# Kernel tuning notes

Hardware: AMD Instinct MI355X
Metric: run time of the kernel (lower is better)

Reference implementation:

```python
import jax, jax.numpy as jnp
import numpy as np

N_CELLS = 50000
HID = 64
DEG = 16
K_NODES = 4  # nodes per cell; cell i owns nodes [4i, 4i+4)
SP = 3


def setup_inputs() -> dict:
    key = jax.random.key(0)
    ks = jax.random.split(key, 12)
    s = 1.0 / np.sqrt(HID)
    inp = {
        'features': jax.random.normal(ks[0], (N_CELLS, HID), jnp.float32),
        'positions': jax.random.normal(ks[1], (K_NODES * N_CELLS, SP), jnp.float32),
        'neighbors': jax.random.randint(ks[2], (N_CELLS, DEG), 0, N_CELLS, jnp.int32),
        # message MLP: Linear(2H+1 -> H), SiLU, Linear(H -> H)
        'W1': jax.random.normal(ks[3], (2 * HID + 1, HID), jnp.float32) * s,
        'b1': jnp.zeros((HID,), jnp.float32),
        'W2': jax.random.normal(ks[4], (HID, HID), jnp.float32) * s,
        'b2': jnp.zeros((HID,), jnp.float32),
        # update MLP: Linear(H + H -> H), SiLU, Linear(H -> H)
        'Wu1': jax.random.normal(ks[5], (2 * HID, HID), jnp.float32) * s,
        'bu1': jnp.zeros((HID,), jnp.float32),
        'Wu2': jax.random.normal(ks[6], (HID, HID), jnp.float32) * s,
        'bu2': jnp.zeros((HID,), jnp.float32),
    }
    return inp


def reference(features, positions, neighbors, W1, b1, W2, b2, Wu1, bu1, Wu2, bu2):
    N, H = features.shape
    # centroid of each cell's owned nodes (cell i -> nodes [K*i, K*i+K))
    cent = positions.reshape(N, K_NODES, SP).mean(axis=1)          # [N, sp]
    fj = features[neighbors]                                       # [N, D, H]
    cj = cent[neighbors]                                           # [N, D, sp]
    # centroid-distance geometric invariant per (cell, neighbor) pair
    geom = jnp.linalg.norm(cent[:, None, :] - cj, axis=-1, keepdims=True)  # [N, D, 1]
    fi = jnp.broadcast_to(features[:, None, :], fj.shape)          # [N, D, H]
    x = jnp.concatenate([fi, fj, geom], axis=-1)                   # [N, D, 2H+1]
    h = jax.nn.silu(x @ W1 + b1) @ W2 + b2                         # [N, D, H]
    msg = h.mean(axis=1)                                           # mean over neighbors
    u = jnp.concatenate([features, msg], axis=-1)                  # [N, 2H]
    upd = jax.nn.silu(u @ Wu1 + bu1) @ Wu2 + bu2
    updated_features = features + upd
    return updated_features, positions
```

## Files before the change

### kernel.cpp

```cpp
#include <hip/hip_runtime.h>
#include <hip/hip_bf16.h>


#define DEG 16

typedef __attribute__((ext_vector_type(8))) short short8;
typedef __attribute__((ext_vector_type(4))) float f32x4;
typedef uint2 uint2_a __attribute__((may_alias));
typedef uint4 uint4_a __attribute__((may_alias));
typedef unsigned short ushort_a __attribute__((may_alias));

union HbRd { uint4_a u; short8 s; };
union Frag { short8 s; uint4 u; };

__device__ __forceinline__ unsigned cvtpk2(float lo, float hi) {
  float2 p; p.x = lo; p.y = hi;
  __hip_bfloat162 h = __float22bfloat162_rn(p);
  union { __hip_bfloat162 b; unsigned u; } cv; cv.b = h;
  return cv.u;
}
__device__ __forceinline__ unsigned short f2bf1(float f) {
  __hip_bfloat16 h = __float2bfloat16(f);
  union { __hip_bfloat16 b; unsigned short u; } cv; cv.b = h;
  return cv.u;
}
__device__ __forceinline__ float bf2f(unsigned bits16) {
  return __uint_as_float(bits16 << 16);
}
__device__ __forceinline__ float silu(float h) {
  return h / (1.f + __expf(-h));
}
__device__ __forceinline__ float silu_fast(float h) {
  return h * __builtin_amdgcn_rcpf(1.f + __expf(-h));
}

#define EARLY_LOADS(T, NJ, G, XF)                                              \
  {                                                                            \
    _Pragma("unroll")                                                          \
    for (int i_ = 0; i_ < 4; ++i_) {                                           \
      const int cs_ = __builtin_amdgcn_readfirstlane((T) * 16 + wid * 4 + i_); \
      NJ[i_] = nbr[cs_ * DEG + l15];                                           \
    }                                                                          \
    _Pragma("unroll")                                                          \
    for (int i_ = 0; i_ < 4; ++i_) {                                           \
      const int cs_ = __builtin_amdgcn_readfirstlane((T) * 16 + wid * 4 + i_); \
      const float4 ci_ = cent4c[cs_];                                          \
      const float4 cj_ = cent4c[NJ[i_]];                                       \
      const float dx_ = ci_.x - cj_.x, dy_ = ci_.y - cj_.y,                    \
                  dz_ = ci_.z - cj_.z;                                         \
      G[i_] = sqrtf(dx_ * dx_ + dy_ * dy_ + dz_ * dz_);                        \
    }                                                                          \
    const int crE_ = (T) * 16 + l15;                                           \
    _Pragma("unroll")                                                          \
    for (int kk_ = 0; kk_ < 2; ++kk_) {                                        \
      const float4 f0_ =                                                       \
          *(const float4*)(feat + crE_ * 64 + kk_ * 32 + quad * 8);            \
      const float4 f1_ =                                                       \
          *(const float4*)(feat + crE_ * 64 + kk_ * 32 + quad * 8 + 4);        \
      Frag v_;                                                                 \
      v_.u.x = cvtpk2(f0_.x, f0_.y);                                           \
      v_.u.y = cvtpk2(f0_.z, f0_.w);                                           \
      v_.u.z = cvtpk2(f1_.x, f1_.y);                                           \
      v_.u.w = cvtpk2(f1_.z, f1_.w);                                           \
      XF[kk_] = v_.s;                                                          \
    }                                                                          \
  }

__global__ __launch_bounds__(256) void prep_aux_kernel(
    const float* __restrict__ feat,
    const float* __restrict__ pos,
    const float* __restrict__ W1, const float* __restrict__ W2,
    const float* __restrict__ Wu1, const float* __restrict__ Wu2,
    float* __restrict__ outpos, float* __restrict__ cent4,
    unsigned short* __restrict__ w1pq, unsigned short* __restrict__ w2t,
    unsigned short* __restrict__ wu1t, unsigned short* __restrict__ wu2b,
    unsigned char* __restrict__ Q8)
{
  __shared__ unsigned short w1q[4096];

  if (blockIdx.x < 782) {
    const int tid  = threadIdx.x;
    const int lane = tid & 63;
    const int wid  = tid >> 6;
    const int quad = lane >> 4;
    const int l15  = lane & 15;

    {
      const int k  = tid >> 2;
      const int mq = tid & 3;
      const int kk = k >> 5, q = (k >> 3) & 3, j = k & 7;
      const int sbase = ((mq * 2 + kk) * 4 + q) * 128 + j;
      const float* src = W1 + 4096 + tid * 16;
      #pragma unroll
      for (int c = 0; c < 4; ++c) {
        const float4 f = *(const float4*)(src + c * 4);
        const unsigned p01 = cvtpk2(f.x, f.y);
        const unsigned p23 = cvtpk2(f.z, f.w);
        w1q[sbase + (c * 4 + 0) * 8] = (unsigned short)p01;
        w1q[sbase + (c * 4 + 1) * 8] = (unsigned short)(p01 >> 16);
        w1q[sbase + (c * 4 + 2) * 8] = (unsigned short)p23;
        w1q[sbase + (c * 4 + 3) * 8] = (unsigned short)(p23 >> 16);
      }
    }

    const int tile = blockIdx.x * 4 + wid;
    const bool act = (tile < 3125);
    const int  tt  = act ? tile : 3124;
    const int  cr  = tt * 16 + l15;

    short8 xf[2];
    #pragma unroll
    for (int kk = 0; kk < 2; ++kk) {
      const float4 f0 = *(const float4*)(feat + cr * 64 + kk * 32 + quad * 8);
      const float4 f1 = *(const float4*)(feat + cr * 64 + kk * 32 + quad * 8 + 4);
      Frag v;
      v.u.x = cvtpk2(f0.x, f0.y);
      v.u.y = cvtpk2(f0.z, f0.w);
      v.u.z = cvtpk2(f1.x, f1.y);
      v.u.w = cvtpk2(f1.z, f1.w);
      xf[kk] = v.s;
    }

    __syncthreads();

    short8 wf[4][2];
    #pragma unroll
    for (int m = 0; m < 4; ++m)
      #pragma unroll
      for (int kk = 0; kk < 2; ++kk)
        wf[m][kk] = *(const short8*)(w1q + (((m * 2 + kk) * 4 + quad) << 7) + l15 * 8);

    f32x4 acc[4] = {};
    #pragma unroll
    for (int kk = 0; kk < 2; ++kk)
      #pragma unroll
      for (int m = 0; m < 4; ++m)
        acc[m] = __builtin_amdgcn_mfma_f32_16x16x32_bf16(wf[m][kk], xf[kk], acc[m], 0, 0, 0);

    if (act) {
      #pragma unroll
      for (int m = 0; m < 4; ++m) {
        int w = __builtin_amdgcn_cvt_pk_fp8_f32(acc[m][0], acc[m][1], 0, false);
        w = __builtin_amdgcn_cvt_pk_fp8_f32(acc[m][2], acc[m][3], w, true);
        *(unsigned int*)(Q8 + cr * 64 + m * 16 + quad * 4) = (unsigned)w;
      }
    }
  } else {
    const int t = (blockIdx.x - 782) * 256 + threadIdx.x;
    if (t < 150000) {
      ((float4*)outpos)[t] = ((const float4*)pos)[t];
    } else if (t < 174576) {
      const int r = t - 150000;
      if (r < 8192) {
        const int j = r & 7, l = (r >> 3) & 15, q = (r >> 7) & 3;
        const int f = r >> 9, kk = f & 1, mt = f >> 1;
        const int k = kk * 32 + q * 8 + j;
        const int m = mt * 16 + l;
        w1pq[r] = f2bf1(
            (m < 64) ? W1[k * 64 + m] : W1[(k + 64) * 64 + (m - 64)]);
      } else if (r < 12288) {
        const int s = r - 8192;
        const int j = s & 7, l = (s >> 3) & 15, q = (s >> 7) & 3;
        const int f = s >> 9, kk = f & 1, mt = f >> 1;
        const int k = kk * 32 + q * 8 + j;
        w2t[s] = f2bf1(W2[k * 64 + mt * 16 + l]);
      } else if (r < 20480) {
        const int s = r - 12288;
        const int j = s & 7, l = (s >> 3) & 15, q = (s >> 7) & 3;
        const int f = s >> 9, kk = f & 3, mt = f >> 2;
        const int k = kk * 32 + q * 8 + j;
        wu1t[s] = f2bf1(Wu1[k * 64 + mt * 16 + l]);
      } else {
        const int s = r - 20480;
        const int j = s & 7, l = (s >> 3) & 15, q = (s >> 7) & 3;
        const int f = s >> 9, kk = f & 1, nt = f >> 1;
        const int k = kk * 32 + q * 8 + j;
        wu2b[s] = f2bf1(Wu2[k * 64 + nt * 16 + l]);
      }
    } else if (t < 224576) {
      const int i = t - 174576;
      const float4* pp = (const float4*)(pos + 12 * i);
      const float4 a = pp[0], b = pp[1], c = pp[2];
      float4 o;
      o.x = (a.x + a.w + b.z + c.y) * 0.25f;
      o.y = (a.y + b.x + b.w + c.z) * 0.25f;
      o.z = (a.z + b.y + c.x + c.w) * 0.25f;
      o.w = 0.f;
      ((float4*)cent4)[i] = o;
    }
  }
}

__global__ __launch_bounds__(256) void msg_tail_kernel(
    const unsigned char* __restrict__ Q8,
    const float4* __restrict__ cent4c,
    const int* __restrict__ nbr,
    const float* __restrict__ feat,
    const unsigned short* __restrict__ w1pq,
    const unsigned short* __restrict__ w2t,
    const unsigned short* __restrict__ wu1t,
    const unsigned short* __restrict__ wu2b,
    const float* __restrict__ b1, const float* __restrict__ W1,
    const float* __restrict__ b2, const float* __restrict__ bu1,
    const float* __restrict__ bu2,
    float* __restrict__ outf)
{
  __shared__ uint4 smem[432];
  char* sT  = (char*)smem;
  char* Msg = sT + 2304;
  char* Hb  = sT + 4608;

  const int lane = threadIdx.x & 63;
  const int wid  = threadIdx.x >> 6;
  const int quad = lane >> 4;
  const int l15  = lane & 15;
  const int tile = blockIdx.x;
  const int cr   = tile * 16 + l15;

  const float b1l = b1[lane];
  const float wl  = W1[8192 + lane];

  short8 wpf[2], w2f[2], wu1f[4], wu2f[2];
  #pragma unroll
  for (int kk = 0; kk < 2; ++kk)
    wpf[kk]  = *(const short8*)(w1pq + (((wid * 2 + kk) * 4 + quad) << 7) + l15 * 8);
  #pragma unroll
  for (int kk = 0; kk < 2; ++kk)
    w2f[kk]  = *(const short8*)(w2t  + (((wid * 2 + kk) * 4 + quad) << 7) + l15 * 8);
  #pragma unroll
  for (int kk = 0; kk < 4; ++kk)
    wu1f[kk] = *(const short8*)(wu1t + (((wid * 4 + kk) * 4 + quad) << 7) + l15 * 8);
  #pragma unroll
  for (int kk = 0; kk < 2; ++kk)
    wu2f[kk] = *(const short8*)(wu2b + (((wid * 2 + kk) * 4 + quad) << 7) + l15 * 8);

  const f32x4 b2f  = *(const f32x4*)(b2  + wid * 16 + quad * 4);
  const f32x4 bu1f = *(const f32x4*)(bu1 + wid * 16 + quad * 4);
  const float bu2v = bu2[wid * 16 + l15];

  int nj[4]; float g[4]; short8 xf[2];
  EARLY_LOADS(tile, nj, g, xf);

  unsigned qA[16], qB[16];
  #pragma unroll
  for (int d = 0; d < 16; ++d) {
    const int nd = __builtin_amdgcn_readlane(nj[0], d);
    qA[d] = Q8[nd * 64 + lane];
  }
  #pragma unroll
  for (int d = 0; d < 16; ++d) {
    const int nd = __builtin_amdgcn_readlane(nj[1], d);
    qB[d] = Q8[nd * 64 + lane];
  }

  {
    f32x4 accp = {};
    #pragma unroll
    for (int kk = 0; kk < 2; ++kk)
      accp = __builtin_amdgcn_mfma_f32_16x16x32_bf16(wpf[kk], xf[kk], accp, 0, 0, 0);
    uint2 pk;
    pk.x = cvtpk2(accp[0], accp[1]);
    pk.y = cvtpk2(accp[2], accp[3]);
    *(uint2_a*)(sT + l15 * 144 + wid * 32 + quad * 8) = pk;
  }

  __syncthreads();

  #pragma unroll
  for (int i = 0; i < 4; ++i) {
    unsigned (&qc)[16] = (i & 1) ? qB : qA;
    const float pcb =
        bf2f(((const ushort_a*)(sT + (wid * 4 + i) * 144))[lane]) + b1l;
    float acc = 0.f;
    #pragma unroll
    for (int d = 0; d < 16; ++d) {
      const float gd = __uint_as_float(
          __builtin_amdgcn_readlane((int)__float_as_uint(g[i]), d));
      const float qv = __builtin_amdgcn_cvt_f32_fp8((int)qc[d], 0);
      acc += silu_fast(pcb + qv + gd * wl);
    }
    if (i < 2) {
      #pragma unroll
      for (int d = 0; d < 16; ++d) {
        const int nd = __builtin_amdgcn_readlane(nj[i + 2], d);
        qc[d] = Q8[nd * 64 + lane];
      }
    }
    ((ushort_a*)(sT + (wid * 4 + i) * 144))[lane] = f2bf1(acc * 0.0625f);
  }

  __syncthreads();

  {
    f32x4 accm = {};
    #pragma unroll
    for (int kk = 0; kk < 2; ++kk) {
      HbRd t; t.u = *(const uint4_a*)(sT + l15 * 144 + kk * 64 + quad * 16);
      accm = __builtin_amdgcn_mfma_f32_16x16x32_bf16(w2f[kk], t.s, accm, 0, 0, 0);
    }
    uint2 pk;
    pk.x = cvtpk2(accm[0] + b2f[0], accm[1] + b2f[1]);
    pk.y = cvtpk2(accm[2] + b2f[2], accm[3] + b2f[3]);
    *(uint2_a*)(Msg + l15 * 144 + wid * 32 + quad * 8) = pk;
  }
  __syncthreads();

  {
    f32x4 accu = {};
    #pragma unroll
    for (int kk = 0; kk < 4; ++kk) {
      short8 bf;
      if (kk < 2) {
        bf = xf[kk];
      } else {
        HbRd t; t.u = *(const uint4_a*)(Msg + l15 * 144 + (kk - 2) * 64 + quad * 16);
        bf = t.s;
      }
      accu = __builtin_amdgcn_mfma_f32_16x16x32_bf16(wu1f[kk], bf, accu, 0, 0, 0);
    }
    float sv[4];
    #pragma unroll
    for (int rg = 0; rg < 4; ++rg)
      sv[rg] = silu(accu[rg] + bu1f[rg]);
    uint2 pk;
    pk.x = cvtpk2(sv[0], sv[1]);
    pk.y = cvtpk2(sv[2], sv[3]);
    *(uint2_a*)(Hb + l15 * 144 + wid * 32 + quad * 8) = pk;
  }
  __syncthreads();

  {
    f32x4 acc2 = {};
    #pragma unroll
    for (int kk = 0; kk < 2; ++kk) {
      HbRd t; t.u = *(const uint4_a*)(Hb + l15 * 144 + kk * 64 + quad * 16);
      acc2 = __builtin_amdgcn_mfma_f32_16x16x32_bf16(t.s, wu2f[kk], acc2, 0, 0, 0);
    }
    #pragma unroll
    for (int rg = 0; rg < 4; ++rg) {
      const int row = tile * 16 + quad * 4 + rg;
      const int col = wid * 16 + l15;
      outf[row * 64 + col] = feat[row * 64 + col] + acc2[rg] + bu2v;
    }
  }
}

extern "C" void kernel_launch(void* const* d_in, const int* in_sizes, int n_in,
                              void* d_out, int out_size, void* d_ws, size_t ws_size,
                              hipStream_t stream)
{
  const float* feat = (const float*)d_in[0];
  const float* pos  = (const float*)d_in[1];
  const int*   nbr  = (const int*)d_in[2];
  const float* W1   = (const float*)d_in[3];
  const float* b1   = (const float*)d_in[4];
  const float* W2   = (const float*)d_in[5];
  const float* b2   = (const float*)d_in[6];
  const float* Wu1  = (const float*)d_in[7];
  const float* bu1  = (const float*)d_in[8];
  const float* Wu2  = (const float*)d_in[9];
  const float* bu2  = (const float*)d_in[10];
  float* out = (float*)d_out;

  unsigned char*  Q8    = (unsigned char*)((char*)d_ws + 12800000);
  float*          cent4 = (float*)((char*)d_ws + 25600000);
  unsigned short* w1pq  = (unsigned short*)((char*)d_ws + 26400000);
  unsigned short* w2t   = (unsigned short*)((char*)d_ws + 26416384);
  unsigned short* wu1t  = (unsigned short*)((char*)d_ws + 26424576);
  unsigned short* wu2b  = (unsigned short*)((char*)d_ws + 26440960);

  prep_aux_kernel<<<1660, 256, 0, stream>>>(feat, pos, W1, W2, Wu1, Wu2,
                                            out + 3200000, cent4,
                                            w1pq, w2t, wu1t, wu2b, Q8);
  msg_tail_kernel<<<3125, 256, 0, stream>>>(Q8, (const float4*)cent4, nbr, feat,
                                            w1pq, w2t, wu1t, wu2b,
                                            b1, W1, b2, bu1, bu2, out);
}
```

Measured before the change: 124.0 us.

## Restructure message kernel to one wave per 16-cell tile with per-lane neighbor loop

```diff
diff --git a/kernel.cpp b/kernel.cpp
--- a/kernel.cpp
+++ b/kernel.cpp
@@ -24,47 +24,12 @@
   union { __hip_bfloat16 b; unsigned short u; } cv; cv.b = h;
   return cv.u;
 }
-__device__ __forceinline__ float bf2f(unsigned bits16) {
-  return __uint_as_float(bits16 << 16);
-}
 __device__ __forceinline__ float silu(float h) {
   return h / (1.f + __expf(-h));
 }
 __device__ __forceinline__ float silu_fast(float h) {
   return h * __builtin_amdgcn_rcpf(1.f + __expf(-h));
 }
-
-#define EARLY_LOADS(T, NJ, G, XF)                                              \
-  {                                                                            \
-    _Pragma("unroll")                                                          \
-    for (int i_ = 0; i_ < 4; ++i_) {                                           \
-      const int cs_ = __builtin_amdgcn_readfirstlane((T) * 16 + wid * 4 + i_); \
-      NJ[i_] = nbr[cs_ * DEG + l15];                                           \
-    }                                                                          \
-    _Pragma("unroll")                                                          \
-    for (int i_ = 0; i_ < 4; ++i_) {                                           \
-      const int cs_ = __builtin_amdgcn_readfirstlane((T) * 16 + wid * 4 + i_); \
-      const float4 ci_ = cent4c[cs_];                                          \
-      const float4 cj_ = cent4c[NJ[i_]];                                       \
-      const float dx_ = ci_.x - cj_.x, dy_ = ci_.y - cj_.y,                    \
-                  dz_ = ci_.z - cj_.z;                                         \
-      G[i_] = sqrtf(dx_ * dx_ + dy_ * dy_ + dz_ * dz_);                        \
-    }                                                                          \
-    const int crE_ = (T) * 16 + l15;                                           \
-    _Pragma("unroll")                                                          \
-    for (int kk_ = 0; kk_ < 2; ++kk_) {                                        \
-      const float4 f0_ =                                                       \
-          *(const float4*)(feat + crE_ * 64 + kk_ * 32 + quad * 8);            \
-      const float4 f1_ =                                                       \
-          *(const float4*)(feat + crE_ * 64 + kk_ * 32 + quad * 8 + 4);        \
-      Frag v_;                                                                 \
-      v_.u.x = cvtpk2(f0_.x, f0_.y);                                           \
-      v_.u.y = cvtpk2(f0_.z, f0_.w);                                           \
-      v_.u.z = cvtpk2(f1_.x, f1_.y);                                           \
-      v_.u.w = cvtpk2(f1_.z, f1_.w);                                           \
-      XF[kk_] = v_.s;                                                          \
-    }                                                                          \
-  }
 
 __global__ __launch_bounds__(256) void prep_aux_kernel(
     const float* __restrict__ feat,
@@ -191,7 +156,7 @@
   }
 }
 
-__global__ __launch_bounds__(256) void msg_tail_kernel(
+__global__ __launch_bounds__(64, 3) void msg_tail_kernel(
     const unsigned char* __restrict__ Q8,
     const float4* __restrict__ cent4c,
     const int* __restrict__ nbr,
@@ -205,142 +170,168 @@
     const float* __restrict__ bu2,
     float* __restrict__ outf)
 {
-  __shared__ uint4 smem[432];
-  char* sT  = (char*)smem;
-  char* Msg = sT + 2304;
-  char* Hb  = sT + 4608;
-
-  const int lane = threadIdx.x & 63;
-  const int wid  = threadIdx.x >> 6;
+  __shared__ __align__(16) char sT[2304];
+  __shared__ __align__(16) char Msg[2304];
+  __shared__ __align__(16) char Hb[2304];
+
+  const int lane = threadIdx.x;
   const int quad = lane >> 4;
   const int l15  = lane & 15;
   const int tile = blockIdx.x;
   const int cr   = tile * 16 + l15;
 
-  const float b1l = b1[lane];
-  const float wl  = W1[8192 + lane];
-
-  short8 wpf[2], w2f[2], wu1f[4], wu2f[2];
-  #pragma unroll
-  for (int kk = 0; kk < 2; ++kk)
-    wpf[kk]  = *(const short8*)(w1pq + (((wid * 2 + kk) * 4 + quad) << 7) + l15 * 8);
-  #pragma unroll
-  for (int kk = 0; kk < 2; ++kk)
-    w2f[kk]  = *(const short8*)(w2t  + (((wid * 2 + kk) * 4 + quad) << 7) + l15 * 8);
-  #pragma unroll
-  for (int kk = 0; kk < 4; ++kk)
-    wu1f[kk] = *(const short8*)(wu1t + (((wid * 4 + kk) * 4 + quad) << 7) + l15 * 8);
-  #pragma unroll
-  for (int kk = 0; kk < 2; ++kk)
-    wu2f[kk] = *(const short8*)(wu2b + (((wid * 2 + kk) * 4 + quad) << 7) + l15 * 8);
-
-  const f32x4 b2f  = *(const f32x4*)(b2  + wid * 16 + quad * 4);
-  const f32x4 bu1f = *(const f32x4*)(bu1 + wid * 16 + quad * 4);
-  const float bu2v = bu2[wid * 16 + l15];
-
-  int nj[4]; float g[4]; short8 xf[2];
-  EARLY_LOADS(tile, nj, g, xf);
-
-  unsigned qA[16], qB[16];
+  int nj[16];
+  #pragma unroll
+  for (int c = 0; c < 4; ++c) {
+    const int4 v = *(const int4*)(nbr + cr * 16 + c * 4);
+    nj[c * 4 + 0] = v.x; nj[c * 4 + 1] = v.y;
+    nj[c * 4 + 2] = v.z; nj[c * 4 + 3] = v.w;
+  }
+  const float4 ci = cent4c[cr];
+
+  short8 xf[2];
+  #pragma unroll
+  for (int kk = 0; kk < 2; ++kk) {
+    const float4 f0 = *(const float4*)(feat + cr * 64 + kk * 32 + quad * 8);
+    const float4 f1 = *(const float4*)(feat + cr * 64 + kk * 32 + quad * 8 + 4);
+    Frag v;
+    v.u.x = cvtpk2(f0.x, f0.y);
+    v.u.y = cvtpk2(f0.z, f0.w);
+    v.u.z = cvtpk2(f1.x, f1.y);
+    v.u.w = cvtpk2(f1.z, f1.w);
+    xf[kk] = v.s;
+  }
+
+  f32x4 wlv[4];
+  #pragma unroll
+  for (int mt = 0; mt < 4; ++mt)
+    wlv[mt] = *(const f32x4*)(W1 + 8192 + mt * 16 + quad * 4);
+
+  f32x4 pc[4];
+  #pragma unroll
+  for (int mt = 0; mt < 4; ++mt) {
+    f32x4 a = {};
+    #pragma unroll
+    for (int kk = 0; kk < 2; ++kk) {
+      const short8 w =
+          *(const short8*)(w1pq + (((mt * 2 + kk) * 4 + quad) << 7) + l15 * 8);
+      a = __builtin_amdgcn_mfma_f32_16x16x32_bf16(w, xf[kk], a, 0, 0, 0);
+    }
+    const f32x4 b1v = *(const f32x4*)(b1 + mt * 16 + quad * 4);
+    #pragma unroll
+    for (int rg = 0; rg < 4; ++rg) a[rg] += b1v[rg];
+    pc[mt] = a;
+  }
+
+  f32x4 sa[4] = {};
+  unsigned q[2][4];
+  float4 cj[2];
+  #pragma unroll
+  for (int mt = 0; mt < 4; ++mt)
+    q[0][mt] = *(const unsigned*)(Q8 + nj[0] * 64 + mt * 16 + quad * 4);
+  cj[0] = cent4c[nj[0]];
+
   #pragma unroll
   for (int d = 0; d < 16; ++d) {
-    const int nd = __builtin_amdgcn_readlane(nj[0], d);
-    qA[d] = Q8[nd * 64 + lane];
-  }
-  #pragma unroll
-  for (int d = 0; d < 16; ++d) {
-    const int nd = __builtin_amdgcn_readlane(nj[1], d);
-    qB[d] = Q8[nd * 64 + lane];
-  }
-
-  {
-    f32x4 accp = {};
-    #pragma unroll
-    for (int kk = 0; kk < 2; ++kk)
-      accp = __builtin_amdgcn_mfma_f32_16x16x32_bf16(wpf[kk], xf[kk], accp, 0, 0, 0);
+    const int cur = d & 1, nxt = cur ^ 1;
+    if (d < 15) {
+      #pragma unroll
+      for (int mt = 0; mt < 4; ++mt)
+        q[nxt][mt] =
+            *(const unsigned*)(Q8 + nj[d + 1] * 64 + mt * 16 + quad * 4);
+      cj[nxt] = cent4c[nj[d + 1]];
+    }
+    const float dx = ci.x - cj[cur].x, dy = ci.y - cj[cur].y,
+                dz = ci.z - cj[cur].z;
+    const float g = sqrtf(dx * dx + dy * dy + dz * dz);
+    #pragma unroll
+    for (int mt = 0; mt < 4; ++mt) {
+      const int qw = (int)q[cur][mt];
+      const float qv0 = __builtin_amdgcn_cvt_f32_fp8(qw, 0);
+      const float qv1 = __builtin_amdgcn_cvt_f32_fp8(qw, 1);
+      const float qv2 = __builtin_amdgcn_cvt_f32_fp8(qw, 2);
+      const float qv3 = __builtin_amdgcn_cvt_f32_fp8(qw, 3);
+      sa[mt][0] += silu_fast(pc[mt][0] + qv0 + g * wlv[mt][0]);
+      sa[mt][1] += silu_fast(pc[mt][1] + qv1 + g * wlv[mt][1]);
+      sa[mt][2] += silu_fast(pc[mt][2] + qv2 + g * wlv[mt][2]);
+      sa[mt][3] += silu_fast(pc[mt][3] + qv3 + g * wlv[mt][3]);
+    }
+  }
+
+  #pragma unroll
+  for (int mt = 0; mt < 4; ++mt) {
     uint2 pk;
-    pk.x = cvtpk2(accp[0], accp[1]);
-    pk.y = cvtpk2(accp[2], accp[3]);
-    *(uint2_a*)(sT + l15 * 144 + wid * 32 + quad * 8) = pk;
-  }
-
+    pk.x = cvtpk2(sa[mt][0] * 0.0625f, sa[mt][1] * 0.0625f);
+    pk.y = cvtpk2(sa[mt][2] * 0.0625f, sa[mt][3] * 0.0625f);
+    *(uint2_a*)(sT + l15 * 144 + mt * 32 + quad * 8) = pk;
+  }
   __syncthreads();
 
   #pragma unroll
-  for (int i = 0; i < 4; ++i) {
-    unsigned (&qc)[16] = (i & 1) ? qB : qA;
-    const float pcb =
-        bf2f(((const ushort_a*)(sT + (wid * 4 + i) * 144))[lane]) + b1l;
-    float acc = 0.f;
-    #pragma unroll
-    for (int d = 0; d < 16; ++d) {
-      const float gd = __uint_as_float(
-          __builtin_amdgcn_readlane((int)__float_as_uint(g[i]), d));
-      const float qv = __builtin_amdgcn_cvt_f32_fp8((int)qc[d], 0);
-      acc += silu_fast(pcb + qv + gd * wl);
-    }
-    if (i < 2) {
-      #pragma unroll
-      for (int d = 0; d < 16; ++d) {
-        const int nd = __builtin_amdgcn_readlane(nj[i + 2], d);
-        qc[d] = Q8[nd * 64 + lane];
+  for (int mt = 0; mt < 4; ++mt) {
+    f32x4 a = {};
+    #pragma unroll
+    for (int kk = 0; kk < 2; ++kk) {
+      const short8 w =
+          *(const short8*)(w2t + (((mt * 2 + kk) * 4 + quad) << 7) + l15 * 8);
+      HbRd t; t.u = *(const uint4_a*)(sT + l15 * 144 + kk * 64 + quad * 16);
+      a = __builtin_amdgcn_mfma_f32_16x16x32_bf16(w, t.s, a, 0, 0, 0);
+    }
+    const f32x4 b2v = *(const f32x4*)(b2 + mt * 16 + quad * 4);
+    uint2 pk;
+    pk.x = cvtpk2(a[0] + b2v[0], a[1] + b2v[1]);
+    pk.y = cvtpk2(a[2] + b2v[2], a[3] + b2v[3]);
+    *(uint2_a*)(Msg + l15 * 144 + mt * 32 + quad * 8) = pk;
+  }
+  __syncthreads();
+
+  #pragma unroll
+  for (int mt = 0; mt < 4; ++mt) {
+    f32x4 a = {};
+    #pragma unroll
+    for (int kk = 0; kk < 4; ++kk) {
+      const short8 w =
+          *(const short8*)(wu1t + (((mt * 4 + kk) * 4 + quad) << 7) + l15 * 8);
+      short8 bfr;
+      if (kk < 2) {
+        bfr = xf[kk];
+      } else {
+        HbRd t;
+        t.u = *(const uint4_a*)(Msg + l15 * 144 + (kk - 2) * 64 + quad * 16);
+        bfr = t.s;
       }
-    }
-    ((ushort_a*)(sT + (wid * 4 + i) * 144))[lane] = f2bf1(acc * 0.0625f);
-  }
-
-  __syncthreads();
-
-  {
-    f32x4 accm = {};
-    #pragma unroll
-    for (int kk = 0; kk < 2; ++kk) {
-      HbRd t; t.u = *(const uint4_a*)(sT + l15 * 144 + kk * 64 + quad * 16);
-      accm = __builtin_amdgcn_mfma_f32_16x16x32_bf16(w2f[kk], t.s, accm, 0, 0, 0);
-    }
-    uint2 pk;
-    pk.x = cvtpk2(accm[0] + b2f[0], accm[1] + b2f[1]);
-    pk.y = cvtpk2(accm[2] + b2f[2], accm[3] + b2f[3]);
-    *(uint2_a*)(Msg + l15 * 144 + wid * 32 + quad * 8) = pk;
-  }
-  __syncthreads();
-
-  {
-    f32x4 accu = {};
-    #pragma unroll
-    for (int kk = 0; kk < 4; ++kk) {
-      short8 bf;
-      if (kk < 2) {
-        bf = xf[kk];
-      } else {
-        HbRd t; t.u = *(const uint4_a*)(Msg + l15 * 144 + (kk - 2) * 64 + quad * 16);
-        bf = t.s;
-      }
-      accu = __builtin_amdgcn_mfma_f32_16x16x32_bf16(wu1f[kk], bf, accu, 0, 0, 0);
-    }
+      a = __builtin_amdgcn_mfma_f32_16x16x32_bf16(w, bfr, a, 0, 0, 0);
+    }
+    const f32x4 buv = *(const f32x4*)(bu1 + mt * 16 + quad * 4);
     float sv[4];
     #pragma unroll
-    for (int rg = 0; rg < 4; ++rg)
-      sv[rg] = silu(accu[rg] + bu1f[rg]);
+    for (int rg = 0; rg < 4; ++rg) sv[rg] = silu(a[rg] + buv[rg]);
     uint2 pk;
     pk.x = cvtpk2(sv[0], sv[1]);
     pk.y = cvtpk2(sv[2], sv[3]);
-    *(uint2_a*)(Hb + l15 * 144 + wid * 32 + quad * 8) = pk;
+    *(uint2_a*)(Hb + l15 * 144 + mt * 32 + quad * 8) = pk;
   }
   __syncthreads();
 
-  {
-    f32x4 acc2 = {};
+  HbRd hf[2];
+  #pragma unroll
+  for (int kk = 0; kk < 2; ++kk)
+    hf[kk].u = *(const uint4_a*)(Hb + l15 * 144 + kk * 64 + quad * 16);
+  #pragma unroll
+  for (int nt = 0; nt < 4; ++nt) {
+    f32x4 a = {};
     #pragma unroll
     for (int kk = 0; kk < 2; ++kk) {
-      HbRd t; t.u = *(const uint4_a*)(Hb + l15 * 144 + kk * 64 + quad * 16);
-      acc2 = __builtin_amdgcn_mfma_f32_16x16x32_bf16(t.s, wu2f[kk], acc2, 0, 0, 0);
-    }
+      const short8 w =
+          *(const short8*)(wu2b + (((nt * 2 + kk) * 4 + quad) << 7) + l15 * 8);
+      a = __builtin_amdgcn_mfma_f32_16x16x32_bf16(hf[kk].s, w, a, 0, 0, 0);
+    }
+    const float bv = bu2[nt * 16 + l15];
     #pragma unroll
     for (int rg = 0; rg < 4; ++rg) {
       const int row = tile * 16 + quad * 4 + rg;
-      const int col = wid * 16 + l15;
-      outf[row * 64 + col] = feat[row * 64 + col] + acc2[rg] + bu2v;
+      const int col = nt * 16 + l15;
+      outf[row * 64 + col] = feat[row * 64 + col] + a[rg] + bv;
     }
   }
 }
@@ -372,7 +363,7 @@
   prep_aux_kernel<<<1660, 256, 0, stream>>>(feat, pos, W1, W2, Wu1, Wu2,
                                             out + 3200000, cent4,
                                             w1pq, w2t, wu1t, wu2b, Q8);
-  msg_tail_kernel<<<3125, 256, 0, stream>>>(Q8, (const float4*)cent4, nbr, feat,
-                                            w1pq, w2t, wu1t, wu2b,
-                                            b1, W1, b2, bu1, bu2, out);
-}
+  msg_tail_kernel<<<3125, 64, 0, stream>>>(Q8, (const float4*)cent4, nbr, feat,
+                                           w1pq, w2t, wu1t, wu2b,
+                                           b1, W1, b2, bu1, bu2, out);
+}
```

Measured after the change: 130.6 us. 1.05x slower.
